# Kernel optimization log

Hardware: AMD Instinct MI355X
Metric: run time of the kernel (lower is better)

The kernel has to match this reference:

```python
import jax, jax.numpy as jnp
import numpy as np

EPS_ATTN = 1e-5   # attention denominator eps (module eps)
EPS_LN = 1e-5     # nn.LayerNorm default eps


def _prime(x, proj):
    # Performer FAVOR+ hyperbolic positive features.
    # x: (B,H,L,dh), proj: (dh,m) -> (B,H,L,2m)
    dn = x.shape[-1] ** -0.25
    xn = dn * x
    d = jnp.einsum('bhld,dm->bhlm', xn, proj)
    diag = 0.5 * jnp.sum(xn * xn, axis=-1, keepdims=True)
    return jnp.concatenate([jnp.exp(d - diag), jnp.exp(-d - diag)], axis=-1)


def setup_inputs() -> dict:
    L, B, H, DH, DM, M = 2048, 4, 8, 64, 512, 256
    key = jax.random.key(0)
    k0, k1, k2 = jax.random.split(key, 3)
    h = jax.random.normal(k0, (L, B, DM), jnp.float32)
    w_qkv = jax.random.normal(k1, (H * 3 * DH, DM), jnp.float32) / np.sqrt(DM)
    w_o = jax.random.normal(k2, (DM, H * DH), jnp.float32) / np.sqrt(H * DH)
    ln_gamma = jnp.ones((DM,), jnp.float32)
    ln_beta = jnp.zeros((DM,), jnp.float32)
    # Gaussian orthogonal random matrix (blockwise QR), rows scaled by sqrt(dh)
    rng = np.random.default_rng(0)
    blocks = []
    for _ in range(M // DH):
        g = rng.standard_normal((DH, DH)).astype(np.float32)
        q, _ = np.linalg.qr(g)
        blocks.append(q.T)
    pm = np.concatenate(blocks, axis=0) * np.sqrt(DH)  # (M, DH)
    proj_matrix = jnp.asarray(pm.T.astype(np.float32))  # (DH, M)
    return {"h": h, "w_qkv": w_qkv, "w_o": w_o,
            "ln_gamma": ln_gamma, "ln_beta": ln_beta,
            "proj_matrix": proj_matrix}


def _forward(h, w_qkv, w_o, ln_gamma, ln_beta, proj_matrix):
    L, B, DM = h.shape
    DH, M = proj_matrix.shape
    H = w_qkv.shape[0] // (3 * DH)
    scale = DH ** -0.5

    qkv = (h @ w_qkv.T).reshape(L, B, H, 3 * DH)
    q, k, v = jnp.split(qkv, 3, axis=-1)
    q = jnp.transpose(q, (1, 2, 0, 3))  # (B,H,L,dh)
    k = jnp.transpose(k, (1, 2, 0, 3))
    v = jnp.transpose(v, (1, 2, 0, 3))

    qp = _prime(q, proj_matrix)  # (B,H,L,2M)
    kp = _prime(k, proj_matrix)
    kp = kp / jnp.sum(kp, axis=-1, keepdims=True)
    qp = qp / jnp.sum(qp, axis=-1, keepdims=True)

    den_acc = jnp.cumsum(kp, axis=2)
    denom = jnp.einsum('bhlm,bhlm->bhl', den_acc, qp)[..., None]  # (B,H,L,1)

    # fast_weight_sum: W_t = W_{t-1} + k_t v_t^T ; out_t = q_t @ W_t
    def step(W, xs):
        qt, kt, vt = xs  # (B,H,2M), (B,H,2M), (B,H,dh)
        W = W + kt[..., :, None] * vt[..., None, :]
        out = jnp.einsum('bhm,bhmd->bhd', qt, W)
        return W, out

    W0 = jnp.zeros((B, H, 2 * M, DH), h.dtype)
    xs = (jnp.transpose(qp, (2, 0, 1, 3)),
          jnp.transpose(kp, (2, 0, 1, 3)),
          jnp.transpose(v, (2, 0, 1, 3)))
    _, out = jax.lax.scan(step, W0, xs)  # (L,B,H,dh)
    out = jnp.transpose(out, (1, 2, 0, 3))  # (B,H,L,dh)

    out = scale * out / (denom + EPS_ATTN)
    out = jnp.transpose(out, (0, 2, 1, 3)).reshape(B, L, H * DH)  # (B,L,H*dh)
    out = jnp.swapaxes(out, 0, 1)  # (L,B,H*dh)

    attn_out = out @ w_o.T
    x = h + attn_out
    mu = jnp.mean(x, axis=-1, keepdims=True)
    var = jnp.mean((x - mu) ** 2, axis=-1, keepdims=True)
    return (x - mu) / jnp.sqrt(var + EPS_LN) * ln_gamma + ln_beta


def reference(h, w_qkv, w_o, ln_gamma, ln_beta, proj_matrix):
    return _forward(h, w_qkv, w_o, ln_gamma, ln_beta, proj_matrix)
```

## Files before the change

### kernel.cpp

```cpp
#include <hip/hip_runtime.h>
#include <hip/hip_fp16.h>
#include <math.h>

#define LSEQ 2048
#define NB 4
#define NH 8
#define DMID 512
#define CHK 128
#define SCALE 0.125f
#define DN 0.35355339059327373f
#define DN2 0.125f
#define EPS_ATTN 1e-5f
#define EPS_LN 1e-5f

typedef _Float16 f16x8 __attribute__((ext_vector_type(8)));
typedef _Float16 f16x4 __attribute__((ext_vector_type(4)));
typedef float f32x4 __attribute__((ext_vector_type(4)));

__device__ __forceinline__ void cvt16(const float* __restrict__ p,
                                      _Float16* __restrict__ dst) {
  float4 a = *(const float4*)p, b = *(const float4*)(p + 4);
  float4 c = *(const float4*)(p + 8), d = *(const float4*)(p + 12);
  f16x8 t0 = {(_Float16)a.x, (_Float16)a.y, (_Float16)a.z, (_Float16)a.w,
              (_Float16)b.x, (_Float16)b.y, (_Float16)b.z, (_Float16)b.w};
  f16x8 t1 = {(_Float16)c.x, (_Float16)c.y, (_Float16)c.z, (_Float16)c.w,
              (_Float16)d.x, (_Float16)d.y, (_Float16)d.z, (_Float16)d.w};
  *(f16x8*)dst = t0;
  *(f16x8*)(dst + 8) = t1;
}

__global__ void k_diag(float* out, int n, float val) {
  int i = blockIdx.x * 256 + threadIdx.x;
  if (i < n) out[i] = val;
}

__global__ __launch_bounds__(256) void k_ptr(const float* __restrict__ proj,
                                             __half* __restrict__ projT) {
  int e = blockIdx.x * 256 + threadIdx.x;
  int n = e >> 6, k = e & 63;
  projT[e] = __float2half_rn(proj[k * 256 + n] * DN);
}

__global__ __launch_bounds__(256) void k_qkv(
    const float* __restrict__ A, const float* __restrict__ Wq,
    __half* __restrict__ q, __half* __restrict__ k, __half* __restrict__ v) {
  __shared__ __align__(16) char smem[34816];
  _Float16* Ah = (_Float16*)smem;
  _Float16* Bh = (_Float16*)(smem + 10240);
  _Float16* Oh = (_Float16*)smem;

  const int tid = threadIdx.x;
  const int row0 = blockIdx.x * 128;
  const int col0 = blockIdx.y * 128;
  const int lane = tid & 63, wv = tid >> 6;
  const int ln15 = lane & 15, quad = lane >> 4;
  const int m0 = wv * 32;
  const int srow = tid >> 1, sc = (tid & 1) * 16;

  f32x4 Cacc[2][8];
  const f32x4 z4 = {0.f, 0.f, 0.f, 0.f};
#pragma unroll
  for (int mi = 0; mi < 2; ++mi)
#pragma unroll
    for (int nt = 0; nt < 8; ++nt) Cacc[mi][nt] = z4;

  for (int kt = 0; kt < DMID; kt += 32) {
    cvt16(A + (size_t)(row0 + srow) * DMID + kt + sc, &Ah[srow * 40 + sc]);
    cvt16(Wq + (size_t)(col0 + srow) * DMID + kt + sc, &Bh[srow * 40 + sc]);
    __syncthreads();
    f16x8 a0 = *(const f16x8*)&Ah[(m0 + ln15) * 40 + quad * 8];
    f16x8 a1 = *(const f16x8*)&Ah[(m0 + 16 + ln15) * 40 + quad * 8];
#pragma unroll
    for (int nt = 0; nt < 8; ++nt) {
      f16x8 bf = *(const f16x8*)&Bh[(nt * 16 + ln15) * 40 + quad * 8];
      Cacc[0][nt] = __builtin_amdgcn_mfma_f32_16x16x32_f16(a0, bf, Cacc[0][nt], 0, 0, 0);
      Cacc[1][nt] = __builtin_amdgcn_mfma_f32_16x16x32_f16(a1, bf, Cacc[1][nt], 0, 0, 0);
    }
    __syncthreads();
  }
#pragma unroll
  for (int mi = 0; mi < 2; ++mi)
#pragma unroll
    for (int nt = 0; nt < 8; ++nt)
#pragma unroll
      for (int r = 0; r < 4; ++r)
        Oh[(m0 + mi * 16 + quad * 4 + r) * 136 + nt * 16 + ln15] =
            (_Float16)Cacc[mi][nt][r];
  __syncthreads();
  const int tr = tid >> 4, tc = tid & 15;
  const int col = col0 + tc * 8;
  const int hh = col / 192;
  const int rem = col - hh * 192;
  const int t = rem >> 6;
  const int d0 = rem & 63;
  __half* dstb = (t == 0) ? q : ((t == 1) ? k : v);
#pragma unroll
  for (int i = 0; i < 8; ++i) {
    int lrow = tr * 8 + i;
    int grow = row0 + lrow;
    int l = grow >> 2, bb = grow & 3;
    f16x8 val = *(const f16x8*)&Oh[lrow * 136 + tc * 8];
    *(f16x8*)((_Float16*)dstb + (((size_t)(bb * NH + hh) * LSEQ + l) << 6) + d0) = val;
  }
}

__global__ __launch_bounds__(256) void k_dgemm(
    const __half* __restrict__ qsrc, const __half* __restrict__ ksrc,
    const __half* __restrict__ projT, __half* __restrict__ dqd,
    __half* __restrict__ dkd, float2* __restrict__ nq,
    float2* __restrict__ nk) {
  __shared__ __align__(16) char smem[37888];
  _Float16* Bt = (_Float16*)smem;
  float* g_l  = (float*)(smem + 36864);
  float* ps_l = (float*)(smem + 37376);
  _Float16* Oh = (_Float16*)smem;

  const int tid = threadIdx.x;
  const __half* src = blockIdx.y ? ksrc : qsrc;
  __half* dst = blockIdx.y ? dkd : dqd;
  float2* nrm = blockIdx.y ? nk : nq;
  const size_t r0 = (size_t)blockIdx.x * 128;

  const int lane = tid & 63, wv = tid >> 6;
  const int ln15 = lane & 15, quad = lane >> 4;
  const int m0 = wv * 32;

#pragma unroll
  for (int it = 0; it < 8; ++it) {
    int e = it * 256 + tid;
    int n = e >> 3, seg = e & 7;
    *(f16x8*)&Bt[n * 72 + seg * 8] =
        *(const f16x8*)((const _Float16*)projT + n * 64 + seg * 8);
  }

  f16x8 afrag[2][2];
  float ss[2] = {0.f, 0.f};
#pragma unroll
  for (int mi = 0; mi < 2; ++mi) {
    const _Float16* rp =
        (const _Float16*)src + (r0 + m0 + mi * 16 + ln15) * 64;
#pragma unroll
    for (int ks = 0; ks < 2; ++ks) {
      f16x8 x8 = *(const f16x8*)(rp + ks * 32 + quad * 8);
      afrag[mi][ks] = x8;
#pragma unroll
      for (int j = 0; j < 8; ++j) {
        float xv = (float)x8[j];
        ss[mi] = fmaf(xv, xv, ss[mi]);
      }
    }
    ss[mi] += __shfl_xor(ss[mi], 16);
    ss[mi] += __shfl_xor(ss[mi], 32);
  }
  if (quad == 0) {
    g_l[m0 + ln15] = 0.5f * DN2 * ss[0];
    g_l[m0 + 16 + ln15] = 0.5f * DN2 * ss[1];
  }
  __syncthreads();

  f32x4 Cacc[2][16];
  const f32x4 z4 = {0.f, 0.f, 0.f, 0.f};
#pragma unroll
  for (int mi = 0; mi < 2; ++mi)
#pragma unroll
    for (int nt = 0; nt < 16; ++nt) Cacc[mi][nt] = z4;

#pragma unroll
  for (int ks = 0; ks < 2; ++ks) {
    f16x8 a0 = afrag[0][ks];
    f16x8 a1 = afrag[1][ks];
#pragma unroll
    for (int nt = 0; nt < 16; ++nt) {
      f16x8 bf = *(const f16x8*)&Bt[(nt * 16 + ln15) * 72 + ks * 32 + quad * 8];
      Cacc[0][nt] = __builtin_amdgcn_mfma_f32_16x16x32_f16(a0, bf, Cacc[0][nt], 0, 0, 0);
      Cacc[1][nt] = __builtin_amdgcn_mfma_f32_16x16x32_f16(a1, bf, Cacc[1][nt], 0, 0, 0);
    }
  }

  float gv[2][4], pp[2][4];
#pragma unroll
  for (int mi = 0; mi < 2; ++mi)
#pragma unroll
    for (int r = 0; r < 4; ++r) {
      gv[mi][r] = g_l[m0 + mi * 16 + quad * 4 + r];
      pp[mi][r] = 0.f;
    }
#pragma unroll
  for (int mi = 0; mi < 2; ++mi)
#pragma unroll
    for (int nt = 0; nt < 16; ++nt)
#pragma unroll
      for (int r = 0; r < 4; ++r) {
        float d = Cacc[mi][nt][r];
        pp[mi][r] += __expf(d - gv[mi][r]) + __expf(-d - gv[mi][r]);
      }
#pragma unroll
  for (int mi = 0; mi < 2; ++mi)
#pragma unroll
    for (int r = 0; r < 4; ++r) {
      float p = pp[mi][r];
      p += __shfl_xor(p, 1); p += __shfl_xor(p, 2);
      p += __shfl_xor(p, 4); p += __shfl_xor(p, 8);
      if (ln15 == 0) ps_l[m0 + mi * 16 + quad * 4 + r] = p;
    }

#pragma unroll
  for (int hf = 0; hf < 2; ++hf) {
    __syncthreads();
#pragma unroll
    for (int mi = 0; mi < 2; ++mi)
#pragma unroll
      for (int nt2 = 0; nt2 < 8; ++nt2) {
        int nt = hf * 8 + nt2;
#pragma unroll
        for (int r = 0; r < 4; ++r)
          Oh[(m0 + mi * 16 + quad * 4 + r) * 136 + nt2 * 16 + ln15] =
              (_Float16)Cacc[mi][nt][r];
      }
    __syncthreads();
#pragma unroll
    for (int it = 0; it < 8; ++it) {
      int e = it * 256 + tid;
      int row = e >> 4, seg = e & 15;
      *(f16x8*)((_Float16*)dst + (r0 + row) * 256 + hf * 128 + seg * 8) =
          *(const f16x8*)&Oh[row * 136 + seg * 8];
    }
  }
  if (tid < 128) nrm[r0 + tid] = make_float2(g_l[tid], 1.0f / ps_l[tid]);
}

__global__ __launch_bounds__(256) void k_kv(
    const __half* __restrict__ dk, const float2* __restrict__ nk,
    const __half* __restrict__ v, __half* __restrict__ KVt,
    float* __restrict__ Ks) {
  __shared__ __align__(16) char smem[53248];
  _Float16* kpT = (_Float16*)smem;
  _Float16* Vt  = (_Float16*)(smem + 34816);
  float* gk = (float*)(smem + 52224);
  float* ik = (float*)(smem + 52736);
  _Float16* Oh2 = (_Float16*)smem;

  const int tid = threadIdx.x;
  const int cidx = blockIdx.x;
  const int i0 = blockIdx.y * 128;
  const float fsign = (i0 < 256) ? 1.f : -1.f;
  const int m0col = (i0 < 256) ? i0 : i0 - 256;
  const size_t rowbase = (size_t)cidx * CHK;

  if (tid < 128) {
    float2 n = nk[rowbase + tid];
    gk[tid] = n.x; ik[tid] = n.y;
  }
  __syncthreads();

  {
    const int srow = tid >> 1;
    const int scol = (tid & 1) * 64;
    float g = gk[srow], ivs = ik[srow];
    const _Float16* src =
        (const _Float16*)dk + (rowbase + srow) * 256 + m0col + scol;
#pragma unroll
    for (int it = 0; it < 8; ++it) {
      f16x8 d8 = *(const f16x8*)(src + it * 8);
#pragma unroll
      for (int j = 0; j < 8; ++j)
        kpT[(scol + it * 8 + j) * 136 + srow] =
            (_Float16)(__expf(fsign * (float)d8[j] - g) * ivs);
    }
  }
  {
    int s = tid & 127, dq0 = (tid >> 7) * 32;
    const _Float16* vsrc = (const _Float16*)v + (rowbase + s) * 64 + dq0;
#pragma unroll
    for (int b8 = 0; b8 < 4; ++b8) {
      f16x8 v8 = ((const f16x8*)vsrc)[b8];
#pragma unroll
      for (int j = 0; j < 8; ++j)
        Vt[(dq0 + b8 * 8 + j) * 136 + s] = v8[j];
    }
  }
  __syncthreads();

  const int lane = tid & 63, wv = tid >> 6;
  const int ln15 = lane & 15, quad = lane >> 4;
  const int m0 = wv * 32;

  f32x4 Cacc[2][4], Kacc[2];
  const f32x4 z4 = {0.f, 0.f, 0.f, 0.f};
#pragma unroll
  for (int mi = 0; mi < 2; ++mi) {
#pragma unroll
    for (int nt = 0; nt < 4; ++nt) Cacc[mi][nt] = z4;
    Kacc[mi] = z4;
  }
  f16x8 bone;
#pragma unroll
  for (int j = 0; j < 8; ++j)
    bone[j] = (ln15 == 0) ? (_Float16)1.0f : (_Float16)0.0f;

#pragma unroll
  for (int ks = 0; ks < 4; ++ks) {
    f16x8 a0 = *(const f16x8*)&kpT[(m0 + ln15) * 136 + ks * 32 + quad * 8];
    f16x8 a1 = *(const f16x8*)&kpT[(m0 + 16 + ln15) * 136 + ks * 32 + quad * 8];
#pragma unroll
    for (int nt = 0; nt < 4; ++nt) {
      f16x8 bV = *(const f16x8*)&Vt[(nt * 16 + ln15) * 136 + ks * 32 + quad * 8];
      Cacc[0][nt] = __builtin_amdgcn_mfma_f32_16x16x32_f16(a0, bV, Cacc[0][nt], 0, 0, 0);
      Cacc[1][nt] = __builtin_amdgcn_mfma_f32_16x16x32_f16(a1, bV, Cacc[1][nt], 0, 0, 0);
    }
    Kacc[0] = __builtin_amdgcn_mfma_f32_16x16x32_f16(a0, bone, Kacc[0], 0, 0, 0);
    Kacc[1] = __builtin_amdgcn_mfma_f32_16x16x32_f16(a1, bone, Kacc[1], 0, 0, 0);
  }

  if (ln15 == 0) {
#pragma unroll
    for (int mi = 0; mi < 2; ++mi)
#pragma unroll
      for (int r = 0; r < 4; ++r)
        Ks[(size_t)cidx * 512 + i0 + m0 + mi * 16 + quad * 4 + r] = Kacc[mi][r];
  }
  __syncthreads();
#pragma unroll
  for (int mi = 0; mi < 2; ++mi)
#pragma unroll
    for (int nt = 0; nt < 4; ++nt) {
      f16x4 pack = {(_Float16)Cacc[mi][nt][0], (_Float16)Cacc[mi][nt][1],
                    (_Float16)Cacc[mi][nt][2], (_Float16)Cacc[mi][nt][3]};
      *(f16x4*)&Oh2[(nt * 16 + ln15) * 136 + m0 + mi * 16 + quad * 4] = pack;
    }
  __syncthreads();
  {
    int d = tid >> 2, part = tid & 3;
    _Float16* dstp =
        (_Float16*)KVt + (size_t)cidx * 32768 + d * 512 + i0 + part * 32;
    const _Float16* srcp = &Oh2[d * 136 + part * 32];
#pragma unroll
    for (int j = 0; j < 4; ++j)
      *(f16x8*)(dstp + j * 8) = *(const f16x8*)(srcp + j * 8);
  }
}

__global__ __launch_bounds__(256) void k_scan(__half2* __restrict__ KV2,
                                              float* __restrict__ Ks) {
  const int bh = blockIdx.x;
  const int e0 = blockIdx.y * 2048;
  for (int ee = 0; ee < 8; ++ee) {
    int e = e0 + ee * 256 + threadIdx.x;
    float ax = 0.f, ay = 0.f;
    __half2* p = KV2 + (size_t)bh * 16 * 16384 + e;
#pragma unroll
    for (int c = 0; c < 16; ++c) {
      float2 f = __half22float2(p[(size_t)c * 16384]);
      p[(size_t)c * 16384] = __floats2half2_rn(ax, ay);
      ax += f.x; ay += f.y;
    }
  }
  if (blockIdx.y == 0) {
    for (int ee = 0; ee < 2; ++ee) {
      int i = ee * 256 + threadIdx.x;
      float a = 0.f;
      float* p = Ks + (size_t)bh * 16 * 512 + i;
#pragma unroll
      for (int c = 0; c < 16; ++c) {
        float vv = p[c * 512];
        p[c * 512] = a;
        a += vv;
      }
    }
  }
}

__global__ __launch_bounds__(256, 2) void k_attn(
    const __half* __restrict__ dq, const __half* __restrict__ dk,
    const float2* __restrict__ nq, const float2* __restrict__ nk,
    const __half* __restrict__ v, const __half* __restrict__ KVt,
    const float* __restrict__ Kpre, float* __restrict__ outb) {
  __shared__ __align__(16) char smem[55808];
  float* gq_l   = (float*)(smem);
  float* iq_l   = (float*)(smem + 512);
  float* gk_l   = (float*)(smem + 1024);
  float* ik_l   = (float*)(smem + 1536);
  float* den1_l = (float*)(smem + 2048);
  float* den2_l = (float*)(smem + 2560);
  float* invd_l = (float*)(smem + 3072);
  _Float16* qpT = (_Float16*)(smem + 3584);
  _Float16* kpT = (_Float16*)(smem + 13824);
  _Float16* WT  = (_Float16*)(smem + 24064);
  float*    KpT = (float*)(smem + 29184);
  _Float16* S_h = (_Float16*)(smem + 3584);
  _Float16* Vt  = (_Float16*)(smem + 38400);

  const int tid = threadIdx.x;
  const int cidx = blockIdx.x;
  const int cc = cidx & 15, bh = cidx >> 4;
  const size_t rowb = (size_t)cidx * 128;
  const int lane = tid & 63;
  const int wv = tid >> 6;
  const int ln15 = lane & 15;
  const int quad = lane >> 4;
  const int m0 = wv * 32;

  if (tid < 128) {
    float2 n = nq[rowb + tid];
    gq_l[tid] = n.x; iq_l[tid] = n.y;
    float2 n2 = nk[rowb + tid];
    gk_l[tid] = n2.x; ik_l[tid] = n2.y;
  }
  __syncthreads();

  f32x4 Sacc[2][8], Oacc[2][4], Dacc[2];
  const f32x4 z4 = {0.f, 0.f, 0.f, 0.f};
#pragma unroll
  for (int mi = 0; mi < 2; ++mi) {
#pragma unroll
    for (int nt = 0; nt < 8; ++nt) Sacc[mi][nt] = z4;
#pragma unroll
    for (int nt = 0; nt < 4; ++nt) Oacc[mi][nt] = z4;
    Dacc[mi] = z4;
  }

  const int srow = tid >> 1;
  const int sc = (tid & 1) * 16;

  for (int kt = 0; kt < 512; kt += 32) {
    const float sgn = (kt < 256) ? 1.f : -1.f;
    const int dc0 = ((kt < 256) ? kt : kt - 256) + sc;
    {
      const _Float16* src = (const _Float16*)dq + (rowb + srow) * 256 + dc0;
      float g = gq_l[srow], iv = iq_l[srow];
      f16x8 d0 = *(const f16x8*)(src);
      f16x8 d1 = *(const f16x8*)(src + 8);
      f16x8 t0, t1;
#pragma unroll
      for (int j = 0; j < 8; ++j) {
        t0[j] = (_Float16)(__expf(sgn * (float)d0[j] - g) * iv);
        t1[j] = (_Float16)(__expf(sgn * (float)d1[j] - g) * iv);
      }
      *(f16x8*)&qpT[srow * 40 + sc] = t0;
      *(f16x8*)&qpT[srow * 40 + sc + 8] = t1;
    }
    {
      const _Float16* src = (const _Float16*)dk + (rowb + srow) * 256 + dc0;
      float g = gk_l[srow], iv = ik_l[srow];
      f16x8 d0 = *(const f16x8*)(src);
      f16x8 d1 = *(const f16x8*)(src + 8);
      f16x8 t0, t1;
#pragma unroll
      for (int j = 0; j < 8; ++j) {
        t0[j] = (_Float16)(__expf(sgn * (float)d0[j] - g) * iv);
        t1[j] = (_Float16)(__expf(sgn * (float)d1[j] - g) * iv);
      }
      *(f16x8*)&kpT[srow * 40 + sc] = t0;
      *(f16x8*)&kpT[srow * 40 + sc + 8] = t1;
    }
    {
      int d = tid >> 2, seg = tid & 3;
      *(f16x8*)&WT[d * 40 + seg * 8] =
          *(const f16x8*)((const _Float16*)KVt + (size_t)cidx * 32768 +
                          d * 512 + kt + seg * 8);
    }
    if (tid < 32) KpT[tid] = Kpre[(size_t)cidx * 512 + kt + tid];
    __syncthreads();

    f16x8 a0 = *(const f16x8*)&qpT[(m0 + ln15) * 40 + quad * 8];
    f16x8 a1 = *(const f16x8*)&qpT[(m0 + 16 + ln15) * 40 + quad * 8];
#pragma unroll
    for (int nt = 0; nt < 8; ++nt) {
      f16x8 bf = *(const f16x8*)&kpT[(nt * 16 + ln15) * 40 + quad * 8];
      Sacc[0][nt] = __builtin_amdgcn_mfma_f32_16x16x32_f16(a0, bf, Sacc[0][nt], 0, 0, 0);
      Sacc[1][nt] = __builtin_amdgcn_mfma_f32_16x16x32_f16(a1, bf, Sacc[1][nt], 0, 0, 0);
    }
#pragma unroll
    for (int nt = 0; nt < 4; ++nt) {
      f16x8 bw = *(const f16x8*)&WT[(nt * 16 + ln15) * 40 + quad * 8];
      Oacc[0][nt] = __builtin_amdgcn_mfma_f32_16x16x32_f16(a0, bw, Oacc[0][nt], 0, 0, 0);
      Oacc[1][nt] = __builtin_amdgcn_mfma_f32_16x16x32_f16(a1, bw, Oacc[1][nt], 0, 0, 0);
    }
    {
      f16x8 bk;
#pragma unroll
      for (int j = 0; j < 8; ++j)
        bk[j] = (ln15 == 0) ? (_Float16)KpT[quad * 8 + j] : (_Float16)0.f;
      Dacc[0] = __builtin_amdgcn_mfma_f32_16x16x32_f16(a0, bk, Dacc[0], 0, 0, 0);
      Dacc[1] = __builtin_amdgcn_mfma_f32_16x16x32_f16(a1, bk, Dacc[1], 0, 0, 0);
    }
    __syncthreads();
  }

  if (ln15 == 0) {
#pragma unroll
    for (int mi = 0; mi < 2; ++mi)
#pragma unroll
      for (int r = 0; r < 4; ++r)
        den2_l[m0 + mi * 16 + quad * 4 + r] = Dacc[mi][r];
  }
#pragma unroll
  for (int mi = 0; mi < 2; ++mi) {
    float dp[4] = {0.f, 0.f, 0.f, 0.f};
#pragma unroll
    for (int nt = 0; nt < 8; ++nt) {
      int s = nt * 16 + ln15;
#pragma unroll
      for (int r = 0; r < 4; ++r) {
        int tg = m0 + mi * 16 + quad * 4 + r;
        float vsv = (s <= tg) ? Sacc[mi][nt][r] : 0.f;
        dp[r] += vsv;
        S_h[tg * 136 + s] = (_Float16)vsv;
      }
    }
#pragma unroll
    for (int r = 0; r < 4; ++r) {
      float p = dp[r];
      p += __shfl_xor(p, 1); p += __shfl_xor(p, 2);
      p += __shfl_xor(p, 4); p += __shfl_xor(p, 8);
      if (ln15 == 0) den1_l[m0 + mi * 16 + quad * 4 + r] = p;
    }
  }
  __syncthreads();
  if (tid < 128)
    invd_l[tid] = SCALE / (den1_l[tid] + den2_l[tid] + EPS_ATTN);
  {
    int s = tid & 127, d0v = (tid >> 7) * 32;
    const _Float16* vsrc = (const _Float16*)v + (rowb + s) * 64 + d0v;
    f16x8 v0 = ((const f16x8*)vsrc)[0];
    f16x8 v1 = ((const f16x8*)vsrc)[1];
    f16x8 v2 = ((const f16x8*)vsrc)[2];
    f16x8 v3 = ((const f16x8*)vsrc)[3];
#pragma unroll
    for (int j = 0; j < 8; ++j) {
      Vt[(d0v + j) * 136 + s] = v0[j];
      Vt[(d0v + 8 + j) * 136 + s] = v1[j];
      Vt[(d0v + 16 + j) * 136 + s] = v2[j];
      Vt[(d0v + 24 + j) * 136 + s] = v3[j];
    }
  }
  __syncthreads();
#pragma unroll
  for (int ks = 0; ks < 4; ++ks) {
    f16x8 aS0 = *(const f16x8*)&S_h[(m0 + ln15) * 136 + ks * 32 + quad * 8];
    f16x8 aS1 = *(const f16x8*)&S_h[(m0 + 16 + ln15) * 136 + ks * 32 + quad * 8];
#pragma unroll
    for (int nt = 0; nt < 4; ++nt) {
      f16x8 bV = *(const f16x8*)&Vt[(nt * 16 + ln15) * 136 + ks * 32 + quad * 8];
      Oacc[0][nt] = __builtin_amdgcn_mfma_f32_16x16x32_f16(aS0, bV, Oacc[0][nt], 0, 0, 0);
      Oacc[1][nt] = __builtin_amdgcn_mfma_f32_16x16x32_f16(aS1, bV, Oacc[1][nt], 0, 0, 0);
    }
  }
  const int b = bh >> 3, hh = bh & 7;
  float ivv[2][4];
#pragma unroll
  for (int mi = 0; mi < 2; ++mi)
#pragma unroll
    for (int r = 0; r < 4; ++r)
      ivv[mi][r] = invd_l[m0 + mi * 16 + quad * 4 + r];
#pragma unroll
  for (int mi = 0; mi < 2; ++mi)
#pragma unroll
    for (int nt = 0; nt < 4; ++nt) {
      int dcol = nt * 16 + ln15;
#pragma unroll
      for (int r = 0; r < 4; ++r) {
        int t = m0 + mi * 16 + quad * 4 + r;
        int l = cc * 128 + t;
        outb[((size_t)l * 4 + b) * 512 + hh * 64 + dcol] =
            Oacc[mi][nt][r] * ivv[mi][r];
      }
    }
}

__global__ __launch_bounds__(256) void k_oproj(
    const float* __restrict__ A, const float* __restrict__ Wo,
    const float* __restrict__ hres, float* __restrict__ xout) {
  __shared__ __align__(16) char smem[34816];
  _Float16* Ah = (_Float16*)smem;
  _Float16* Bh = (_Float16*)(smem + 10240);
  _Float16* Oh = (_Float16*)smem;

  const int tid = threadIdx.x;
  const int row0 = blockIdx.x * 128;
  const int col0 = blockIdx.y * 128;
  const int lane = tid & 63, wv = tid >> 6;
  const int ln15 = lane & 15, quad = lane >> 4;
  const int m0 = wv * 32;
  const int srow = tid >> 1, sc = (tid & 1) * 16;

  f32x4 Cacc[2][8];
  const f32x4 z4 = {0.f, 0.f, 0.f, 0.f};
#pragma unroll
  for (int mi = 0; mi < 2; ++mi)
#pragma unroll
    for (int nt = 0; nt < 8; ++nt) Cacc[mi][nt] = z4;

  for (int kt = 0; kt < DMID; kt += 32) {
    cvt16(A + (size_t)(row0 + srow) * DMID + kt + sc, &Ah[srow * 40 + sc]);
    cvt16(Wo + (size_t)(col0 + srow) * DMID + kt + sc, &Bh[srow * 40 + sc]);
    __syncthreads();
    f16x8 a0 = *(const f16x8*)&Ah[(m0 + ln15) * 40 + quad * 8];
    f16x8 a1 = *(const f16x8*)&Ah[(m0 + 16 + ln15) * 40 + quad * 8];
#pragma unroll
    for (int nt = 0; nt < 8; ++nt) {
      f16x8 bf = *(const f16x8*)&Bh[(nt * 16 + ln15) * 40 + quad * 8];
      Cacc[0][nt] = __builtin_amdgcn_mfma_f32_16x16x32_f16(a0, bf, Cacc[0][nt], 0, 0, 0);
      Cacc[1][nt] = __builtin_amdgcn_mfma_f32_16x16x32_f16(a1, bf, Cacc[1][nt], 0, 0, 0);
    }
    __syncthreads();
  }
#pragma unroll
  for (int mi = 0; mi < 2; ++mi)
#pragma unroll
    for (int nt = 0; nt < 8; ++nt)
#pragma unroll
      for (int r = 0; r < 4; ++r)
        Oh[(m0 + mi * 16 + quad * 4 + r) * 136 + nt * 16 + ln15] =
            (_Float16)Cacc[mi][nt][r];
  __syncthreads();
  const int tr = tid >> 4, tc = tid & 15;
#pragma unroll
  for (int i = 0; i < 8; ++i) {
    int lrow = tr * 8 + i;
    int grow = row0 + lrow;
    size_t base = (size_t)grow * 512 + col0 + tc * 8;
    f16x8 o = *(const f16x8*)&Oh[lrow * 136 + tc * 8];
    float4 h0 = *(const float4*)(hres + base);
    float4 h1 = *(const float4*)(hres + base + 4);
    *(float4*)(xout + base) =
        make_float4((float)o[0] + h0.x, (float)o[1] + h0.y,
                    (float)o[2] + h0.z, (float)o[3] + h0.w);
    *(float4*)(xout + base + 4) =
        make_float4((float)o[4] + h1.x, (float)o[5] + h1.y,
                    (float)o[6] + h1.z, (float)o[7] + h1.w);
  }
}

__global__ __launch_bounds__(256) void k_ln(float* __restrict__ x,
                                            const float* __restrict__ g,
                                            const float* __restrict__ bta) {
  __shared__ float ws_[4], wq_[4];
  const int row = blockIdx.x;
  const int tid = threadIdx.x;
  float2 vv = *(const float2*)(x + (size_t)row * 512 + tid * 2);
  float s = vv.x + vv.y;
  float sq = vv.x * vv.x + vv.y * vv.y;
#pragma unroll
  for (int off = 1; off < 64; off <<= 1) {
    s += __shfl_xor(s, off, 64);
    sq += __shfl_xor(sq, off, 64);
  }
  if ((tid & 63) == 0) { ws_[tid >> 6] = s; wq_[tid >> 6] = sq; }
  __syncthreads();
  s = ws_[0] + ws_[1] + ws_[2] + ws_[3];
  sq = wq_[0] + wq_[1] + wq_[2] + wq_[3];
  float mu = s * (1.f / 512.f);
  float var = sq * (1.f / 512.f) - mu * mu;
  float rstd = rsqrtf(var + EPS_LN);
  int c = tid * 2;
  float2 o;
  o.x = (vv.x - mu) * rstd * g[c] + bta[c];
  o.y = (vv.y - mu) * rstd * g[c + 1] + bta[c + 1];
  *(float2*)(x + (size_t)row * 512 + c) = o;
}

extern "C" void kernel_launch(void* const* d_in, const int* in_sizes, int n_in,
                              void* d_out, int out_size, void* d_ws,
                              size_t ws_size, hipStream_t stream) {
  const float* h    = (const float*)d_in[0];
  const float* wqkv = (const float*)d_in[1];
  const float* wo   = (const float*)d_in[2];
  const float* g    = (const float*)d_in[3];
  const float* bta  = (const float*)d_in[4];
  const float* proj = (const float*)d_in[5];
  float* out = (float*)d_out;
  char* wsb = (char*)d_ws;

  __half* q   = (__half*)(wsb + 0);
  __half* kb  = (__half*)(wsb + 8388608);
  __half* vb  = (__half*)(wsb + 16777216);
  __half* dq  = (__half*)(wsb + 25165824);
  __half* dk  = (__half*)(wsb + 58720256);
  float2* nq  = (float2*)(wsb + 92274688);
  float2* nk  = (float2*)(wsb + 92798976);
  __half* KVt = (__half*)(wsb + 93323264);
  float*  Ks  = (float*)(wsb + 126877696);
  __half* pT  = (__half*)(wsb + 127926272);
  float* outb = (float*)(wsb + 0);

  if (ws_size < 127959040ull) {
    float val = 1000.0f + (float)(ws_size >> 20);
    k_diag<<<(out_size + 255) / 256, 256, 0, stream>>>(out, out_size, val);
    return;
  }

  k_ptr  <<<dim3(64), 256, 0, stream>>>(proj, pT);
  k_qkv  <<<dim3(64, 12), 256, 0, stream>>>(h, wqkv, q, kb, vb);
  k_dgemm<<<dim3(512, 2), 256, 0, stream>>>(q, kb, pT, dq, dk, nq, nk);
  k_kv   <<<dim3(512, 4), 256, 0, stream>>>(dk, nk, vb, KVt, Ks);
  k_scan <<<dim3(32, 8), 256, 0, stream>>>((__half2*)KVt, Ks);
  k_attn <<<dim3(512), 256, 0, stream>>>(dq, dk, nq, nk, vb, KVt, Ks, outb);
  k_oproj<<<dim3(64, 4), 256, 0, stream>>>(outb, wo, h, out);
  k_ln   <<<dim3(8192), 256, 0, stream>>>(out, g, bta);
}
```

Measured before the change: 270.8 us.

## Halve row tiles in dgemm and attention kernels to double block count

Both k_dgemm and k_attn now process 64 query rows per block instead of 128, doubling grid size, shrinking LDS and accumulator register use, and raising launch bounds to 4 blocks per CU. In k_attn each half-tile still stages all 128 key rows of the chunk, and the first half skips the upper half of the intra-chunk S·V product because of causality. The aim is higher occupancy and better latency hiding. The cost is duplicated key-feature exp work and duplicated proj/KV tile loads across the two blocks.

```diff
diff --git a/kernel.cpp b/kernel.cpp
--- a/kernel.cpp
+++ b/kernel.cpp
@@ -104,26 +104,26 @@
   }
 }
 
-__global__ __launch_bounds__(256) void k_dgemm(
+__global__ __launch_bounds__(256, 4) void k_dgemm(
     const __half* __restrict__ qsrc, const __half* __restrict__ ksrc,
     const __half* __restrict__ projT, __half* __restrict__ dqd,
     __half* __restrict__ dkd, float2* __restrict__ nq,
     float2* __restrict__ nk) {
-  __shared__ __align__(16) char smem[37888];
+  __shared__ __align__(16) char smem[37376];
   _Float16* Bt = (_Float16*)smem;
   float* g_l  = (float*)(smem + 36864);
-  float* ps_l = (float*)(smem + 37376);
+  float* ps_l = (float*)(smem + 37120);
   _Float16* Oh = (_Float16*)smem;
 
   const int tid = threadIdx.x;
   const __half* src = blockIdx.y ? ksrc : qsrc;
   __half* dst = blockIdx.y ? dkd : dqd;
   float2* nrm = blockIdx.y ? nk : nq;
-  const size_t r0 = (size_t)blockIdx.x * 128;
+  const size_t r0 = (size_t)blockIdx.x * 64;
 
   const int lane = tid & 63, wv = tid >> 6;
   const int ln15 = lane & 15, quad = lane >> 4;
-  const int m0 = wv * 32;
+  const int m0 = wv * 16;
 
 #pragma unroll
   for (int it = 0; it < 8; ++it) {
@@ -133,100 +133,83 @@
         *(const f16x8*)((const _Float16*)projT + n * 64 + seg * 8);
   }
 
-  f16x8 afrag[2][2];
-  float ss[2] = {0.f, 0.f};
-#pragma unroll
-  for (int mi = 0; mi < 2; ++mi) {
-    const _Float16* rp =
-        (const _Float16*)src + (r0 + m0 + mi * 16 + ln15) * 64;
+  f16x8 afrag[2];
+  float ss = 0.f;
+  {
+    const _Float16* rp = (const _Float16*)src + (r0 + m0 + ln15) * 64;
 #pragma unroll
     for (int ks = 0; ks < 2; ++ks) {
       f16x8 x8 = *(const f16x8*)(rp + ks * 32 + quad * 8);
-      afrag[mi][ks] = x8;
+      afrag[ks] = x8;
 #pragma unroll
       for (int j = 0; j < 8; ++j) {
         float xv = (float)x8[j];
-        ss[mi] = fmaf(xv, xv, ss[mi]);
+        ss = fmaf(xv, xv, ss);
       }
     }
-    ss[mi] += __shfl_xor(ss[mi], 16);
-    ss[mi] += __shfl_xor(ss[mi], 32);
-  }
-  if (quad == 0) {
-    g_l[m0 + ln15] = 0.5f * DN2 * ss[0];
-    g_l[m0 + 16 + ln15] = 0.5f * DN2 * ss[1];
-  }
-  __syncthreads();
-
-  f32x4 Cacc[2][16];
+    ss += __shfl_xor(ss, 16);
+    ss += __shfl_xor(ss, 32);
+  }
+  if (quad == 0) g_l[m0 + ln15] = 0.5f * DN2 * ss;
+  __syncthreads();
+
+  f32x4 Cacc[16];
   const f32x4 z4 = {0.f, 0.f, 0.f, 0.f};
 #pragma unroll
-  for (int mi = 0; mi < 2; ++mi)
-#pragma unroll
-    for (int nt = 0; nt < 16; ++nt) Cacc[mi][nt] = z4;
+  for (int nt = 0; nt < 16; ++nt) Cacc[nt] = z4;
 
 #pragma unroll
   for (int ks = 0; ks < 2; ++ks) {
-    f16x8 a0 = afrag[0][ks];
-    f16x8 a1 = afrag[1][ks];
+    f16x8 a0 = afrag[ks];
 #pragma unroll
     for (int nt = 0; nt < 16; ++nt) {
       f16x8 bf = *(const f16x8*)&Bt[(nt * 16 + ln15) * 72 + ks * 32 + quad * 8];
-      Cacc[0][nt] = __builtin_amdgcn_mfma_f32_16x16x32_f16(a0, bf, Cacc[0][nt], 0, 0, 0);
-      Cacc[1][nt] = __builtin_amdgcn_mfma_f32_16x16x32_f16(a1, bf, Cacc[1][nt], 0, 0, 0);
-    }
-  }
-
-  float gv[2][4], pp[2][4];
-#pragma unroll
-  for (int mi = 0; mi < 2; ++mi)
+      Cacc[nt] = __builtin_amdgcn_mfma_f32_16x16x32_f16(a0, bf, Cacc[nt], 0, 0, 0);
+    }
+  }
+
+  float gv[4], pp[4];
+#pragma unroll
+  for (int r = 0; r < 4; ++r) {
+    gv[r] = g_l[m0 + quad * 4 + r];
+    pp[r] = 0.f;
+  }
+#pragma unroll
+  for (int nt = 0; nt < 16; ++nt)
 #pragma unroll
     for (int r = 0; r < 4; ++r) {
-      gv[mi][r] = g_l[m0 + mi * 16 + quad * 4 + r];
-      pp[mi][r] = 0.f;
-    }
-#pragma unroll
-  for (int mi = 0; mi < 2; ++mi)
-#pragma unroll
-    for (int nt = 0; nt < 16; ++nt)
-#pragma unroll
-      for (int r = 0; r < 4; ++r) {
-        float d = Cacc[mi][nt][r];
-        pp[mi][r] += __expf(d - gv[mi][r]) + __expf(-d - gv[mi][r]);
-      }
-#pragma unroll
-  for (int mi = 0; mi < 2; ++mi)
-#pragma unroll
-    for (int r = 0; r < 4; ++r) {
-      float p = pp[mi][r];
-      p += __shfl_xor(p, 1); p += __shfl_xor(p, 2);
-      p += __shfl_xor(p, 4); p += __shfl_xor(p, 8);
-      if (ln15 == 0) ps_l[m0 + mi * 16 + quad * 4 + r] = p;
-    }
+      float d = Cacc[nt][r];
+      pp[r] += __expf(d - gv[r]) + __expf(-d - gv[r]);
+    }
+#pragma unroll
+  for (int r = 0; r < 4; ++r) {
+    float p = pp[r];
+    p += __shfl_xor(p, 1); p += __shfl_xor(p, 2);
+    p += __shfl_xor(p, 4); p += __shfl_xor(p, 8);
+    if (ln15 == 0) ps_l[m0 + quad * 4 + r] = p;
+  }
 
 #pragma unroll
   for (int hf = 0; hf < 2; ++hf) {
     __syncthreads();
 #pragma unroll
-    for (int mi = 0; mi < 2; ++mi)
-#pragma unroll
-      for (int nt2 = 0; nt2 < 8; ++nt2) {
-        int nt = hf * 8 + nt2;
-#pragma unroll
-        for (int r = 0; r < 4; ++r)
-          Oh[(m0 + mi * 16 + quad * 4 + r) * 136 + nt2 * 16 + ln15] =
-              (_Float16)Cacc[mi][nt][r];
-      }
-    __syncthreads();
-#pragma unroll
-    for (int it = 0; it < 8; ++it) {
+    for (int nt2 = 0; nt2 < 8; ++nt2) {
+      int nt = hf * 8 + nt2;
+#pragma unroll
+      for (int r = 0; r < 4; ++r)
+        Oh[(m0 + quad * 4 + r) * 136 + nt2 * 16 + ln15] =
+            (_Float16)Cacc[nt][r];
+    }
+    __syncthreads();
+#pragma unroll
+    for (int it = 0; it < 4; ++it) {
       int e = it * 256 + tid;
       int row = e >> 4, seg = e & 15;
       *(f16x8*)((_Float16*)dst + (r0 + row) * 256 + hf * 128 + seg * 8) =
           *(const f16x8*)&Oh[row * 136 + seg * 8];
     }
   }
-  if (tid < 128) nrm[r0 + tid] = make_float2(g_l[tid], 1.0f / ps_l[tid]);
+  if (tid < 64) nrm[r0 + tid] = make_float2(g_l[tid], 1.0f / ps_l[tid]);
 }
 
 __global__ __launch_bounds__(256) void k_kv(
@@ -370,64 +353,75 @@
   }
 }
 
-__global__ __launch_bounds__(256, 2) void k_attn(
+__global__ __launch_bounds__(256, 4) void k_attn(
     const __half* __restrict__ dq, const __half* __restrict__ dk,
     const float2* __restrict__ nq, const float2* __restrict__ nk,
     const __half* __restrict__ v, const __half* __restrict__ KVt,
     const float* __restrict__ Kpre, float* __restrict__ outb) {
-  __shared__ __align__(16) char smem[55808];
+  __shared__ __align__(16) char smem[40320];
   float* gq_l   = (float*)(smem);
-  float* iq_l   = (float*)(smem + 512);
-  float* gk_l   = (float*)(smem + 1024);
-  float* ik_l   = (float*)(smem + 1536);
-  float* den1_l = (float*)(smem + 2048);
-  float* den2_l = (float*)(smem + 2560);
-  float* invd_l = (float*)(smem + 3072);
-  _Float16* qpT = (_Float16*)(smem + 3584);
-  _Float16* kpT = (_Float16*)(smem + 13824);
-  _Float16* WT  = (_Float16*)(smem + 24064);
-  float*    KpT = (float*)(smem + 29184);
-  _Float16* S_h = (_Float16*)(smem + 3584);
-  _Float16* Vt  = (_Float16*)(smem + 38400);
+  float* iq_l   = (float*)(smem + 256);
+  float* gk_l   = (float*)(smem + 512);
+  float* ik_l   = (float*)(smem + 1024);
+  float* den1_l = (float*)(smem + 1536);
+  float* den2_l = (float*)(smem + 1792);
+  float* invd_l = (float*)(smem + 2048);
+  float* KpT    = (float*)(smem + 2304);
+  _Float16* qpT = (_Float16*)(smem + 2432);
+  _Float16* kpT = (_Float16*)(smem + 7552);
+  _Float16* WT  = (_Float16*)(smem + 17792);
+  _Float16* S_h = (_Float16*)(smem + 2432);
+  _Float16* Vt  = (_Float16*)(smem + 22912);
 
   const int tid = threadIdx.x;
   const int cidx = blockIdx.x;
+  const int th = blockIdx.y;
   const int cc = cidx & 15, bh = cidx >> 4;
   const size_t rowb = (size_t)cidx * 128;
+  const size_t rowt = rowb + th * 64;
   const int lane = tid & 63;
   const int wv = tid >> 6;
   const int ln15 = lane & 15;
   const int quad = lane >> 4;
-  const int m0 = wv * 32;
-
+  const int m0 = wv * 16;
+
+  if (tid < 64) {
+    float2 n = nq[rowt + tid];
+    gq_l[tid] = n.x; iq_l[tid] = n.y;
+  }
   if (tid < 128) {
-    float2 n = nq[rowb + tid];
-    gq_l[tid] = n.x; iq_l[tid] = n.y;
     float2 n2 = nk[rowb + tid];
     gk_l[tid] = n2.x; ik_l[tid] = n2.y;
   }
   __syncthreads();
 
-  f32x4 Sacc[2][8], Oacc[2][4], Dacc[2];
+  f32x4 Sacc[8], Oacc[4], Dacc;
   const f32x4 z4 = {0.f, 0.f, 0.f, 0.f};
 #pragma unroll
-  for (int mi = 0; mi < 2; ++mi) {
-#pragma unroll
-    for (int nt = 0; nt < 8; ++nt) Sacc[mi][nt] = z4;
-#pragma unroll
-    for (int nt = 0; nt < 4; ++nt) Oacc[mi][nt] = z4;
-    Dacc[mi] = z4;
-  }
-
-  const int srow = tid >> 1;
-  const int sc = (tid & 1) * 16;
+  for (int nt = 0; nt < 8; ++nt) Sacc[nt] = z4;
+#pragma unroll
+  for (int nt = 0; nt < 4; ++nt) Oacc[nt] = z4;
+  Dacc = z4;
+
+  const int qrow = tid >> 2, qc = (tid & 3) * 8;
+  const int krow = tid >> 1, kc = (tid & 1) * 16;
 
   for (int kt = 0; kt < 512; kt += 32) {
     const float sgn = (kt < 256) ? 1.f : -1.f;
-    const int dc0 = ((kt < 256) ? kt : kt - 256) + sc;
+    const int dbase = (kt < 256) ? kt : kt - 256;
     {
-      const _Float16* src = (const _Float16*)dq + (rowb + srow) * 256 + dc0;
-      float g = gq_l[srow], iv = iq_l[srow];
+      const _Float16* src = (const _Float16*)dq + (rowt + qrow) * 256 + dbase + qc;
+      float g = gq_l[qrow], iv = iq_l[qrow];
+      f16x8 d0 = *(const f16x8*)(src);
+      f16x8 t0;
+#pragma unroll
+      for (int j = 0; j < 8; ++j)
+        t0[j] = (_Float16)(__expf(sgn * (float)d0[j] - g) * iv);
+      *(f16x8*)&qpT[qrow * 40 + qc] = t0;
+    }
+    {
+      const _Float16* src = (const _Float16*)dk + (rowb + krow) * 256 + dbase + kc;
+      float g = gk_l[krow], iv = ik_l[krow];
       f16x8 d0 = *(const f16x8*)(src);
       f16x8 d1 = *(const f16x8*)(src + 8);
       f16x8 t0, t1;
@@ -436,22 +430,8 @@
         t0[j] = (_Float16)(__expf(sgn * (float)d0[j] - g) * iv);
         t1[j] = (_Float16)(__expf(sgn * (float)d1[j] - g) * iv);
       }
-      *(f16x8*)&qpT[srow * 40 + sc] = t0;
-      *(f16x8*)&qpT[srow * 40 + sc + 8] = t1;
-    }
-    {
-      const _Float16* src = (const _Float16*)dk + (rowb + srow) * 256 + dc0;
-      float g = gk_l[srow], iv = ik_l[srow];
-      f16x8 d0 = *(const f16x8*)(src);
-      f16x8 d1 = *(const f16x8*)(src + 8);
-      f16x8 t0, t1;
-#pragma unroll
-      for (int j = 0; j < 8; ++j) {
-        t0[j] = (_Float16)(__expf(sgn * (float)d0[j] - g) * iv);
-        t1[j] = (_Float16)(__expf(sgn * (float)d1[j] - g) * iv);
-      }
-      *(f16x8*)&kpT[srow * 40 + sc] = t0;
-      *(f16x8*)&kpT[srow * 40 + sc + 8] = t1;
+      *(f16x8*)&kpT[krow * 40 + kc] = t0;
+      *(f16x8*)&kpT[krow * 40 + kc + 8] = t1;
     }
     {
       int d = tid >> 2, seg = tid & 3;
@@ -463,49 +443,42 @@
     __syncthreads();
 
     f16x8 a0 = *(const f16x8*)&qpT[(m0 + ln15) * 40 + quad * 8];
-    f16x8 a1 = *(const f16x8*)&qpT[(m0 + 16 + ln15) * 40 + quad * 8];
 #pragma unroll
     for (int nt = 0; nt < 8; ++nt) {
       f16x8 bf = *(const f16x8*)&kpT[(nt * 16 + ln15) * 40 + quad * 8];
-      Sacc[0][nt] = __builtin_amdgcn_mfma_f32_16x16x32_f16(a0, bf, Sacc[0][nt], 0, 0, 0);
-      Sacc[1][nt] = __builtin_amdgcn_mfma_f32_16x16x32_f16(a1, bf, Sacc[1][nt], 0, 0, 0);
+      Sacc[nt] = __builtin_amdgcn_mfma_f32_16x16x32_f16(a0, bf, Sacc[nt], 0, 0, 0);
     }
 #pragma unroll
     for (int nt = 0; nt < 4; ++nt) {
       f16x8 bw = *(const f16x8*)&WT[(nt * 16 + ln15) * 40 + quad * 8];
-      Oacc[0][nt] = __builtin_amdgcn_mfma_f32_16x16x32_f16(a0, bw, Oacc[0][nt], 0, 0, 0);
-      Oacc[1][nt] = __builtin_amdgcn_mfma_f32_16x16x32_f16(a1, bw, Oacc[1][nt], 0, 0, 0);
+      Oacc[nt] = __builtin_amdgcn_mfma_f32_16x16x32_f16(a0, bw, Oacc[nt], 0, 0, 0);
     }
     {
       f16x8 bk;
 #pragma unroll
       for (int j = 0; j < 8; ++j)
         bk[j] = (ln15 == 0) ? (_Float16)KpT[quad * 8 + j] : (_Float16)0.f;
-      Dacc[0] = __builtin_amdgcn_mfma_f32_16x16x32_f16(a0, bk, Dacc[0], 0, 0, 0);
-      Dacc[1] = __builtin_amdgcn_mfma_f32_16x16x32_f16(a1, bk, Dacc[1], 0, 0, 0);
+      Dacc = __builtin_amdgcn_mfma_f32_16x16x32_f16(a0, bk, Dacc, 0, 0, 0);
     }
     __syncthreads();
   }
 
   if (ln15 == 0) {
 #pragma unroll
-    for (int mi = 0; mi < 2; ++mi)
-#pragma unroll
-      for (int r = 0; r < 4; ++r)
-        den2_l[m0 + mi * 16 + quad * 4 + r] = Dacc[mi][r];
-  }
-#pragma unroll
-  for (int mi = 0; mi < 2; ++mi) {
+    for (int r = 0; r < 4; ++r)
+      den2_l[m0 + quad * 4 + r] = Dacc[r];
+  }
+  {
     float dp[4] = {0.f, 0.f, 0.f, 0.f};
 #pragma unroll
     for (int nt = 0; nt < 8; ++nt) {
       int s = nt * 16 + ln15;
 #pragma unroll
       for (int r = 0; r < 4; ++r) {
-        int tg = m0 + mi * 16 + quad * 4 + r;
-        float vsv = (s <= tg) ? Sacc[mi][nt][r] : 0.f;
+        int tl = m0 + quad * 4 + r;
+        float vsv = (s <= th * 64 + tl) ? Sacc[nt][r] : 0.f;
         dp[r] += vsv;
-        S_h[tg * 136 + s] = (_Float16)vsv;
+        S_h[tl * 136 + s] = (_Float16)vsv;
       }
     }
 #pragma unroll
@@ -513,11 +486,11 @@
       float p = dp[r];
       p += __shfl_xor(p, 1); p += __shfl_xor(p, 2);
       p += __shfl_xor(p, 4); p += __shfl_xor(p, 8);
-      if (ln15 == 0) den1_l[m0 + mi * 16 + quad * 4 + r] = p;
-    }
-  }
-  __syncthreads();
-  if (tid < 128)
+      if (ln15 == 0) den1_l[m0 + quad * 4 + r] = p;
+    }
+  }
+  __syncthreads();
+  if (tid < 64)
     invd_l[tid] = SCALE / (den1_l[tid] + den2_l[tid] + EPS_ATTN);
   {
     int s = tid & 127, d0v = (tid >> 7) * 32;
@@ -535,37 +508,31 @@
     }
   }
   __syncthreads();
-#pragma unroll
-  for (int ks = 0; ks < 4; ++ks) {
+  const int nks = th ? 4 : 2;
+#pragma unroll 4
+  for (int ks = 0; ks < nks; ++ks) {
     f16x8 aS0 = *(const f16x8*)&S_h[(m0 + ln15) * 136 + ks * 32 + quad * 8];
-    f16x8 aS1 = *(const f16x8*)&S_h[(m0 + 16 + ln15) * 136 + ks * 32 + quad * 8];
 #pragma unroll
     for (int nt = 0; nt < 4; ++nt) {
       f16x8 bV = *(const f16x8*)&Vt[(nt * 16 + ln15) * 136 + ks * 32 + quad * 8];
-      Oacc[0][nt] = __builtin_amdgcn_mfma_f32_16x16x32_f16(aS0, bV, Oacc[0][nt], 0, 0, 0);
-      Oacc[1][nt] = __builtin_amdgcn_mfma_f32_16x16x32_f16(aS1, bV, Oacc[1][nt], 0, 0, 0);
+      Oacc[nt] = __builtin_amdgcn_mfma_f32_16x16x32_f16(aS0, bV, Oacc[nt], 0, 0, 0);
     }
   }
   const int b = bh >> 3, hh = bh & 7;
-  float ivv[2][4];
-#pragma unroll
-  for (int mi = 0; mi < 2; ++mi)
-#pragma unroll
-    for (int r = 0; r < 4; ++r)
-      ivv[mi][r] = invd_l[m0 + mi * 16 + quad * 4 + r];
-#pragma unroll
-  for (int mi = 0; mi < 2; ++mi)
-#pragma unroll
-    for (int nt = 0; nt < 4; ++nt) {
-      int dcol = nt * 16 + ln15;
-#pragma unroll
-      for (int r = 0; r < 4; ++r) {
-        int t = m0 + mi * 16 + quad * 4 + r;
-        int l = cc * 128 + t;
-        outb[((size_t)l * 4 + b) * 512 + hh * 64 + dcol] =
-            Oacc[mi][nt][r] * ivv[mi][r];
-      }
-    }
+  float ivv[4];
+#pragma unroll
+  for (int r = 0; r < 4; ++r)
+    ivv[r] = invd_l[m0 + quad * 4 + r];
+#pragma unroll
+  for (int nt = 0; nt < 4; ++nt) {
+    int dcol = nt * 16 + ln15;
+#pragma unroll
+    for (int r = 0; r < 4; ++r) {
+      int tl = m0 + quad * 4 + r;
+      int l = cc * 128 + th * 64 + tl;
+      outb[((size_t)l * 4 + b) * 512 + hh * 64 + dcol] = Oacc[nt][r] * ivv[r];
+    }
+  }
 }
 
 __global__ __launch_bounds__(256) void k_oproj(
@@ -692,10 +659,10 @@
 
   k_ptr  <<<dim3(64), 256, 0, stream>>>(proj, pT);
   k_qkv  <<<dim3(64, 12), 256, 0, stream>>>(h, wqkv, q, kb, vb);
-  k_dgemm<<<dim3(512, 2), 256, 0, stream>>>(q, kb, pT, dq, dk, nq, nk);
+  k_dgemm<<<dim3(1024, 2), 256, 0, stream>>>(q, kb, pT, dq, dk, nq, nk);
   k_kv   <<<dim3(512, 4), 256, 0, stream>>>(dk, nk, vb, KVt, Ks);
   k_scan <<<dim3(32, 8), 256, 0, stream>>>((__half2*)KVt, Ks);
-  k_attn <<<dim3(512), 256, 0, stream>>>(dq, dk, nq, nk, vb, KVt, Ks, outb);
+  k_attn <<<dim3(512, 2), 256, 0, stream>>>(dq, dk, nq, nk, vb, KVt, Ks, outb);
   k_oproj<<<dim3(64, 4), 256, 0, stream>>>(outb, wo, h, out);
   k_ln   <<<dim3(8192), 256, 0, stream>>>(out, g, bta);
 }
```

Result: faster. 259.3 us (-4.3%).
